# Kernel optimization log

Hardware: AMD Instinct MI355X
Metric: run time of the kernel (lower is better)

The kernel has to match this reference:

```python
import jax, jax.numpy as jnp
import numpy as np

N_NODES = 50000
N_EDGES = 800000
R = 3          # relations
D_IN = 96
D_HID = 96
D_OUT = 64


def setup_inputs() -> dict:
    key = jax.random.key(0)
    ks = jax.random.split(key, 10)
    s_in = 1.0 / np.sqrt(D_IN)
    s_hid = 1.0 / np.sqrt(D_HID)
    return {
        "x": jax.random.normal(ks[0], (N_NODES, D_IN), jnp.float32),
        "src": jax.random.randint(ks[1], (R, N_EDGES), 0, N_NODES, jnp.int32),
        "dst": jax.random.randint(ks[2], (R, N_EDGES), 0, N_NODES, jnp.int32),
        "Ws1": jax.random.normal(ks[3], (R, D_IN, D_HID), jnp.float32) * s_in,
        "Wn1": jax.random.normal(ks[4], (R, D_IN, D_HID), jnp.float32) * s_in,
        "b1": jnp.zeros((R, D_HID), jnp.float32),
        "Ws2": jax.random.normal(ks[5], (R, D_HID, D_OUT), jnp.float32) * s_hid,
        "Wn2": jax.random.normal(ks[6], (R, D_HID, D_OUT), jnp.float32) * s_hid,
        "b2": jnp.zeros((R, D_OUT), jnp.float32),
    }


def reference(x, src, dst, Ws1, Wn1, b1, Ws2, Wn2, b2):
    N = x.shape[0]
    # in-degree per relation, clamped to 1 (DGL zero-in-degree convention)
    deg = jax.vmap(lambda d: jax.ops.segment_sum(
        jnp.ones(d.shape[0], x.dtype), d, num_segments=N))(dst)        # [R, N]
    inv_deg = (1.0 / jnp.maximum(deg, 1.0))[..., None]                 # [R, N, 1]

    def sage_layer(h, Ws, Wn, b):
        # gather src feats, mean-aggregate onto dst, per relation
        neigh = jax.vmap(lambda s, d: jax.ops.segment_sum(
            h[s], d, num_segments=N))(src, dst) * inv_deg              # [R, N, Din]
        out = jnp.tanh(
            jnp.einsum('nd,rdh->rnh', h, Ws)
            + jnp.einsum('rnd,rdh->rnh', neigh, Wn)
            + b[:, None, :])                                           # [R, N, H]
        return out.mean(axis=0)  # HeteroGraphConv aggregate='mean'

    h1 = sage_layer(x, Ws1, Wn1, b1)
    return sage_layer(h1, Ws2, Wn2, b2)
```

## Files before the change

### kernel.cpp

```cpp
#include <hip/hip_runtime.h>
#include <hip/hip_bf16.h>

constexpr int NN   = 50000;
constexpr int NE   = 800000;
constexpr int NR   = 3;
constexpr int DIN  = 96;
constexpr int DH   = 96;
constexpr int DOUT = 64;
constexpr int SLOT = 48;
constexpr int ZROW = NN;

constexpr float QS_X   = 127.0f / 5.5f;
constexpr float STEP_X = 5.5f / 127.0f;
constexpr float STEP_H = 1.0f / 127.0f;

constexpr int NBUCK   = 196;
constexpr int LCAP    = 56;
constexpr int P1B     = 256;
constexpr int CHUNK   = NE / P1B;
constexpr int BSTRIDE = 3200;
constexpr int LSTRIDE = 200;

constexpr int SCAT_BLKS = NR * P1B;
constexpr int CONV_BLKS = (NN * 96 + 4095) / 4096;
constexpr int WT_ELEMS  = 2 * NR * DIN * DH + 2 * NR * DH * DOUT;
constexpr int WT_BLKS   = (WT_ELEMS + 511) / 512;
constexpr int PREP_GRID = SCAT_BLKS + CONV_BLKS + WT_BLKS;

typedef __attribute__((ext_vector_type(8))) short bf16x8;
typedef __attribute__((ext_vector_type(4))) float f32x4;
typedef __attribute__((ext_vector_type(4))) unsigned int uint4v;

__device__ __forceinline__ unsigned short f2b(float f) {
    unsigned int u = __float_as_uint(f);
    u += 0x7fffu + ((u >> 16) & 1u);
    return (unsigned short)(u >> 16);
}
__device__ __forceinline__ unsigned int pack2(float lo, float hi) {
    return (unsigned int)f2b(lo) | ((unsigned int)f2b(hi) << 16);
}
__device__ __forceinline__ unsigned int q8u(float f, float s) {
    int v = (int)lrintf(f * s);
    v = v < -127 ? -127 : (v > 127 ? 127 : v);
    return (unsigned int)(v + 128);
}

struct __align__(4) U3 { unsigned int x, y, z; };

__global__ __launch_bounds__(512)
void prep_kernel(const int* __restrict__ src,
                 const int* __restrict__ dst,
                 unsigned int* __restrict__ gbuck,
                 int* __restrict__ glofs,
                 const float* __restrict__ x,
                 unsigned short* __restrict__ xb,
                 unsigned char* __restrict__ xq,
                 unsigned short* __restrict__ h1b,
                 unsigned char* __restrict__ h1q,
                 const float* __restrict__ Ws1, const float* __restrict__ Wn1,
                 const float* __restrict__ Ws2, const float* __restrict__ Wn2,
                 unsigned short* __restrict__ wt)
{
    __shared__ unsigned int lbuf[NBUCK][LCAP];
    __shared__ int lcnt[NBUCK];
    __shared__ int sa[256], sb[256];
    __shared__ int lofs[NBUCK + 1];

    const int bid = blockIdx.x;
    const int tid = threadIdx.x;

    if (bid < SCAT_BLKS) {
        const int r = bid >> 8, c = bid & 255;
        for (int i = tid; i < NBUCK; i += 512) lcnt[i] = 0;
        __syncthreads();

        const int* sr = src + (size_t)r * NE + (size_t)c * CHUNK;
        const int* dr = dst + (size_t)r * NE + (size_t)c * CHUNK;
        for (int i = tid; i < CHUNK; i += 512) {
            int d = dr[i];
            int s = sr[i];
            int b = d >> 8;
            int pos = atomicAdd(&lcnt[b], 1);
            if (pos < LCAP)
                lbuf[b][pos] = ((unsigned int)(d & 255) << 16) | (unsigned int)s;
        }
        __syncthreads();

        if (tid < 256)
            sa[tid] = (tid < NBUCK) ? min(lcnt[tid], LCAP) : 0;
        __syncthreads();
        int* cur = sa; int* nxt = sb;
        for (int st = 1; st < 256; st <<= 1) {
            if (tid < 256) {
                int v = cur[tid];
                if (tid >= st) v += cur[tid - st];
                nxt[tid] = v;
            }
            __syncthreads();
            int* t2 = cur; cur = nxt; nxt = t2;
        }
        if (tid == 0) lofs[0] = 0;
        if (tid < NBUCK) lofs[tid + 1] = cur[tid];
        __syncthreads();

        if (tid < NBUCK + 1) glofs[(size_t)bid * LSTRIDE + tid] = lofs[tid];

        const int w = tid >> 6, l = tid & 63;
        unsigned int* gb = gbuck + (size_t)bid * BSTRIDE;
        for (int b = w; b < NBUCK; b += 8) {
            int cnt = min(lcnt[b], LCAP);
            if (l < cnt) gb[lofs[b] + l] = lbuf[b][l];
        }
    } else if (bid < SCAT_BLKS + CONV_BLKS) {
        const int rb = bid - SCAT_BLKS;
        if (rb == 0) {
            if (tid < 48) {
                reinterpret_cast<unsigned int*>(xb  + (size_t)ZROW * 96)[tid] = 0u;
            } else if (tid >= 64 && tid < 112) {
                reinterpret_cast<unsigned int*>(h1b + (size_t)ZROW * 96)[tid - 64] = 0u;
            } else if (tid >= 128 && tid < 152) {
                reinterpret_cast<unsigned int*>(xq  + (size_t)ZROW * 96)[tid - 128] = 0x80808080u;
            } else if (tid >= 192 && tid < 216) {
                reinterpret_cast<unsigned int*>(h1q + (size_t)ZROW * 96)[tid - 192] = 0x80808080u;
            }
        }
        int i = (rb * 512 + tid) * 8;
        if (i < NN * 96) {
            float4 a = *reinterpret_cast<const float4*>(x + i);
            float4 b = *reinterpret_cast<const float4*>(x + i + 4);
            uint4 o;
            o.x = pack2(a.x, a.y);
            o.y = pack2(a.z, a.w);
            o.z = pack2(b.x, b.y);
            o.w = pack2(b.z, b.w);
            *reinterpret_cast<uint4*>(xb + i) = o;
            unsigned int qlo = q8u(a.x, QS_X) | (q8u(a.y, QS_X) << 8)
                             | (q8u(a.z, QS_X) << 16) | (q8u(a.w, QS_X) << 24);
            unsigned int qhi = q8u(b.x, QS_X) | (q8u(b.y, QS_X) << 8)
                             | (q8u(b.z, QS_X) << 16) | (q8u(b.w, QS_X) << 24);
            unsigned int* q = reinterpret_cast<unsigned int*>(xq + i);
            q[0] = qlo;
            q[1] = qhi;
        }
    } else {
        int g = (bid - SCAT_BLKS - CONV_BLKS) * 512 + tid;
        if (g < WT_ELEMS) {
            constexpr int SZ1 = NR * DIN * DH;
            constexpr int SZ2 = NR * DH * DOUT;
            const float* in;
            int idx, KD, ND;
            if (g < SZ1)                { in = Ws1; idx = g;                 KD = DIN; ND = DH; }
            else if (g < 2 * SZ1)       { in = Wn1; idx = g - SZ1;           KD = DIN; ND = DH; }
            else if (g < 2 * SZ1 + SZ2) { in = Ws2; idx = g - 2 * SZ1;       KD = DH;  ND = DOUT; }
            else                        { in = Wn2; idx = g - 2 * SZ1 - SZ2; KD = DH;  ND = DOUT; }
            int k = idx % KD;
            int rn = idx / KD;
            int n = rn % ND;
            int r = rn / ND;
            wt[g] = f2b(in[((size_t)r * KD + k) * ND + n]);
        }
    }
}

__global__ __launch_bounds__(512)
void bin_build_kernel(const unsigned int* __restrict__ gbuck,
                      const int* __restrict__ glofs,
                      unsigned short* __restrict__ slots,
                      int* __restrict__ deg)
{
    __shared__ unsigned short lslot[256][SLOT];
    __shared__ int lcnt[256];

    const int rb = blockIdx.x;
    const int r  = rb / NBUCK, b = rb - r * NBUCK;
    const int nbase = b * 256;
    int nb = NN - nbase; if (nb > 256) nb = 256;
    const int tid = threadIdx.x;

    unsigned int* ls32i = reinterpret_cast<unsigned int*>(&lslot[0][0]);
    for (int i = tid; i < 256 * SLOT / 2; i += 512) ls32i[i] = 0xC350C350u;
    for (int i = tid; i < 256; i += 512) lcnt[i] = 0;
    __syncthreads();

    const int blk  = tid >> 1;
    const int half = tid & 1;
    const int gblk = r * P1B + blk;
    int o0 = glofs[(size_t)gblk * LSTRIDE + b];
    int o1 = glofs[(size_t)gblk * LSTRIDE + b + 1];
    const unsigned int* run = gbuck + (size_t)gblk * BSTRIDE + o0;
    int cnt = o1 - o0;
    for (int i = half; i < cnt; i += 2) {
        unsigned int e = run[i];
        int nl = e >> 16;
        int pos = atomicAdd(&lcnt[nl], 1);
        if (pos < SLOT) lslot[nl][pos] = (unsigned short)(e & 0xffffu);
    }
    __syncthreads();

    for (int j = tid; j < nb; j += 512) deg[r * NN + nbase + j] = lcnt[j];

    const unsigned int* ls32 = reinterpret_cast<const unsigned int*>(&lslot[0][0]);
    unsigned int* gs32 = reinterpret_cast<unsigned int*>(
        slots + ((size_t)r * NN + nbase) * SLOT);
    const int tot = nb * (SLOT / 2);
    for (int i = tid; i < tot; i += 512) gs32[i] = ls32[i];
}

__global__ __launch_bounds__(256)
void agg_q8_kernel(const unsigned char* __restrict__ Hq,
                   const unsigned short* __restrict__ slots,
                   const int* __restrict__ deg,
                   unsigned int* __restrict__ aggb,
                   float step)
{
    int gid = blockIdx.x * 256 + threadIdx.x;
    int grp = gid >> 3, t = gid & 7;
    if (grp >= NR * NN) return;
    const uint4v* sl4 = reinterpret_cast<const uint4v*>(slots + (size_t)grp * SLOT);
    int e = deg[grp];
    if (e > SLOT) e = SLOT;

    uint4v iv0 = __builtin_nontemporal_load(sl4 + 0);
    uint4v iv1 = __builtin_nontemporal_load(sl4 + 1);
    uint4v iv2 = __builtin_nontemporal_load(sl4 + 2);
    uint4v iv3 = __builtin_nontemporal_load(sl4 + 3);

    const unsigned char* Tb = Hq + 12 * t;
    unsigned int l0 = 0, h0 = 0, l1 = 0, h1 = 0, l2 = 0, h2 = 0;
    const unsigned int M = 0x00FF00FFu;

#define DO8Q(V)                                                                \
    {                                                                          \
        unsigned int i0 = (V).x & 0xffffu, i1 = (V).x >> 16;                   \
        unsigned int i2 = (V).y & 0xffffu, i3 = (V).y >> 16;                   \
        unsigned int i4 = (V).z & 0xffffu, i5 = (V).z >> 16;                   \
        unsigned int i6 = (V).w & 0xffffu, i7 = (V).w >> 16;                   \
        U3 g0 = *reinterpret_cast<const U3*>(Tb + (size_t)i0 * 96);            \
        U3 g1 = *reinterpret_cast<const U3*>(Tb + (size_t)i1 * 96);            \
        U3 g2 = *reinterpret_cast<const U3*>(Tb + (size_t)i2 * 96);            \
        U3 g3 = *reinterpret_cast<const U3*>(Tb + (size_t)i3 * 96);            \
        U3 g4 = *reinterpret_cast<const U3*>(Tb + (size_t)i4 * 96);            \
        U3 g5 = *reinterpret_cast<const U3*>(Tb + (size_t)i5 * 96);            \
        U3 g6 = *reinterpret_cast<const U3*>(Tb + (size_t)i6 * 96);            \
        U3 g7 = *reinterpret_cast<const U3*>(Tb + (size_t)i7 * 96);            \
        l0 += g0.x & M; h0 += (g0.x >> 8) & M;                                 \
        l1 += g0.y & M; h1 += (g0.y >> 8) & M;                                 \
        l2 += g0.z & M; h2 += (g0.z >> 8) & M;                                 \
        l0 += g1.x & M; h0 += (g1.x >> 8) & M;                                 \
        l1 += g1.y & M; h1 += (g1.y >> 8) & M;                                 \
        l2 += g1.z & M; h2 += (g1.z >> 8) & M;                                 \
        l0 += g2.x & M; h0 += (g2.x >> 8) & M;                                 \
        l1 += g2.y & M; h1 += (g2.y >> 8) & M;                                 \
        l2 += g2.z & M; h2 += (g2.z >> 8) & M;                                 \
        l0 += g3.x & M; h0 += (g3.x >> 8) & M;                                 \
        l1 += g3.y & M; h1 += (g3.y >> 8) & M;                                 \
        l2 += g3.z & M; h2 += (g3.z >> 8) & M;                                 \
        l0 += g4.x & M; h0 += (g4.x >> 8) & M;                                 \
        l1 += g4.y & M; h1 += (g4.y >> 8) & M;                                 \
        l2 += g4.z & M; h2 += (g4.z >> 8) & M;                                 \
        l0 += g5.x & M; h0 += (g5.x >> 8) & M;                                 \
        l1 += g5.y & M; h1 += (g5.y >> 8) & M;                                 \
        l2 += g5.z & M; h2 += (g5.z >> 8) & M;                                 \
        l0 += g6.x & M; h0 += (g6.x >> 8) & M;                                 \
        l1 += g6.y & M; h1 += (g6.y >> 8) & M;                                 \
        l2 += g6.z & M; h2 += (g6.z >> 8) & M;                                 \
        l0 += g7.x & M; h0 += (g7.x >> 8) & M;                                 \
        l1 += g7.y & M; h1 += (g7.y >> 8) & M;                                 \
        l2 += g7.z & M; h2 += (g7.z >> 8) & M;                                 \
    }

    int nb8 = (e + 7) >> 3;
    if (nb8 > 0) DO8Q(iv0);
    if (nb8 > 1) DO8Q(iv1);
    if (nb8 > 2) DO8Q(iv2);
    if (nb8 > 3) DO8Q(iv3);
    for (int i = 32; i < e; i += 8) {
        uint4v v = __builtin_nontemporal_load(sl4 + (i >> 3));
        DO8Q(v);
    }
#undef DO8Q

    const int bias = 128 * 8 * nb8;
    const float inv = step / (float)(e > 0 ? e : 1);
    float f0  = (float)((int)(l0 & 0xFFFFu) - bias) * inv;
    float f1  = (float)((int)(h0 & 0xFFFFu) - bias) * inv;
    float f2  = (float)((int)(l0 >> 16)     - bias) * inv;
    float f3  = (float)((int)(h0 >> 16)     - bias) * inv;
    float f4  = (float)((int)(l1 & 0xFFFFu) - bias) * inv;
    float f5  = (float)((int)(h1 & 0xFFFFu) - bias) * inv;
    float f6  = (float)((int)(l1 >> 16)     - bias) * inv;
    float f7  = (float)((int)(h1 >> 16)     - bias) * inv;
    float f8  = (float)((int)(l2 & 0xFFFFu) - bias) * inv;
    float f9  = (float)((int)(h2 & 0xFFFFu) - bias) * inv;
    float f10 = (float)((int)(l2 >> 16)     - bias) * inv;
    float f11 = (float)((int)(h2 >> 16)     - bias) * inv;

    unsigned int* o = aggb + (size_t)grp * 48 + t * 6;
    o[0] = pack2(f0, f1);
    o[1] = pack2(f2, f3);
    o[2] = pack2(f4, f5);
    o[3] = pack2(f6, f7);
    o[4] = pack2(f8, f9);
    o[5] = pack2(f10, f11);
}

template <int NOUT, bool OUT16, int CSPLIT>
__global__ __launch_bounds__(256)
void mfma_layer_kernel(const unsigned short* __restrict__ Hb,
                       const unsigned short* __restrict__ aggb,
                       const unsigned short* __restrict__ Wts,
                       const unsigned short* __restrict__ Wtn,
                       const float* __restrict__ bias,
                       unsigned short* __restrict__ o16,
                       unsigned char* __restrict__ oq8,
                       float* __restrict__ o32)
{
    const int nb   = blockIdx.x / CSPLIT;
    const int cblk = blockIdx.x - nb * CSPLIT;
    const int w    = threadIdx.x >> 6;
    const int l    = threadIdx.x & 63;
    const int n0   = nb * 64 + w * 16;
    const int arow = l & 15, asel = l >> 4;
    int na = n0 + arow;
    if (na > NN - 1) na = NN - 1;

    bf16x8 ax[3], ag[NR][3];
    {
        const unsigned short* xr = Hb + (size_t)na * 96 + asel * 8;
        #pragma unroll
        for (int kb = 0; kb < 3; ++kb)
            ax[kb] = *reinterpret_cast<const bf16x8*>(xr + kb * 32);
        #pragma unroll
        for (int r = 0; r < NR; ++r) {
            const unsigned short* gr = aggb + ((size_t)r * NN + na) * 96 + asel * 8;
            #pragma unroll
            for (int kb = 0; kb < 3; ++kb)
                ag[r][kb] = *reinterpret_cast<const bf16x8*>(gr + kb * 32);
        }
    }

    constexpr int NC  = NOUT / 16;
    constexpr int NCC = NC / CSPLIT;
    #pragma unroll
    for (int ci = 0; ci < NCC; ++ci) {
        const int c = cblk * NCC + ci;
        f32x4 acc[NR];
        #pragma unroll
        for (int r = 0; r < NR; ++r) acc[r] = (f32x4){0.f, 0.f, 0.f, 0.f};

        #pragma unroll
        for (int r = 0; r < NR; ++r) {
            const unsigned short* bs = Wts + ((size_t)r * NOUT + c * 16 + arow) * 96 + asel * 8;
            const unsigned short* bn = Wtn + ((size_t)r * NOUT + c * 16 + arow) * 96 + asel * 8;
            #pragma unroll
            for (int kb = 0; kb < 3; ++kb) {
                acc[r] = __builtin_amdgcn_mfma_f32_16x16x32_bf16(
                    ax[kb], *reinterpret_cast<const bf16x8*>(bs + kb * 32), acc[r], 0, 0, 0);
                acc[r] = __builtin_amdgcn_mfma_f32_16x16x32_bf16(
                    ag[r][kb], *reinterpret_cast<const bf16x8*>(bn + kb * 32), acc[r], 0, 0, 0);
            }
        }

        const int col = c * 16 + arow;
        const float b0 = bias[col];
        const float b1 = bias[NOUT + col];
        const float b2 = bias[2 * NOUT + col];
        #pragma unroll
        for (int j = 0; j < 4; ++j) {
            int node = n0 + asel * 4 + j;
            if (node < NN) {
                float v = (tanhf(acc[0][j] + b0) + tanhf(acc[1][j] + b1)
                         + tanhf(acc[2][j] + b2)) * (1.0f / 3.0f);
                if (OUT16) {
                    o16[(size_t)node * 96 + col] = f2b(v);
                    oq8[(size_t)node * 96 + col] = (unsigned char)q8u(v, 127.0f);
                } else {
                    o32[(size_t)node * DOUT + col] = v;
                }
            }
        }
    }
}

extern "C" void kernel_launch(void* const* d_in, const int* in_sizes, int n_in,
                              void* d_out, int out_size, void* d_ws, size_t ws_size,
                              hipStream_t stream)
{
    const float* x   = (const float*)d_in[0];
    const int*   src = (const int*)d_in[1];
    const int*   dst = (const int*)d_in[2];
    const float* Ws1 = (const float*)d_in[3];
    const float* Wn1 = (const float*)d_in[4];
    const float* b1  = (const float*)d_in[5];
    const float* Ws2 = (const float*)d_in[6];
    const float* Wn2 = (const float*)d_in[7];
    const float* b2  = (const float*)d_in[8];
    float* out = (float*)d_out;

    char* ws = (char*)d_ws;
    size_t o = 0;
    auto alloc = [&](size_t bytes) {
        size_t p = o;
        o += (bytes + 255) & ~(size_t)255;
        return p;
    };
    int* deg = (int*)(ws + alloc((size_t)NR * NN * 4));
    unsigned short* slots = (unsigned short*)(ws + alloc((size_t)NR * NN * SLOT * 2));
    unsigned short* xb = (unsigned short*)(ws + alloc((size_t)(NN + 1) * 96 * 2));
    unsigned char* xq = (unsigned char*)(ws + alloc((size_t)(NN + 1) * 96));
    unsigned short* h1b = (unsigned short*)(ws + alloc((size_t)(NN + 1) * 96 * 2));
    unsigned char* h1q = (unsigned char*)(ws + alloc((size_t)(NN + 1) * 96));
    char* aggregion = ws + alloc((size_t)NR * NN * 96 * 2);
    unsigned short* wt = (unsigned short*)(ws + alloc((size_t)WT_ELEMS * 2));
    unsigned short* wt1s = wt;
    unsigned short* wt1n = wt1s + NR * DIN * DH;
    unsigned short* wt2s = wt1n + NR * DIN * DH;
    unsigned short* wt2n = wt2s + NR * DH * DOUT;

    unsigned int* gbuck = (unsigned int*)aggregion;
    int* glofs = (int*)(aggregion + (size_t)NR * P1B * BSTRIDE * 4);
    unsigned short* aggb = (unsigned short*)aggregion;

    prep_kernel<<<PREP_GRID, 512, 0, stream>>>(
        src, dst, gbuck, glofs, x, xb, xq, h1b, h1q, Ws1, Wn1, Ws2, Wn2, wt);
    bin_build_kernel<<<NR * NBUCK, 512, 0, stream>>>(gbuck, glofs, slots, deg);

    constexpr int AGG_GRID  = (NR * NN * 8 + 255) / 256;
    constexpr int NBLKN     = (NN + 63) / 64;

    agg_q8_kernel<<<AGG_GRID, 256, 0, stream>>>(
        xq, slots, deg, (unsigned int*)aggb, STEP_X);
    mfma_layer_kernel<DH, true, 3><<<NBLKN * 3, 256, 0, stream>>>(
        xb, aggb, wt1s, wt1n, b1, h1b, h1q, (float*)nullptr);

    agg_q8_kernel<<<AGG_GRID, 256, 0, stream>>>(
        h1q, slots, deg, (unsigned int*)aggb, STEP_H);
    mfma_layer_kernel<DOUT, false, 2><<<NBLKN * 2, 256, 0, stream>>>(
        h1b, aggb, wt2s, wt2n, b2, (unsigned short*)nullptr, (unsigned char*)nullptr, out);
}
```

Before: 175.2 us.

## Stage weights in LDS per relation and compute all output columns per block

```diff
diff --git a/kernel.cpp b/kernel.cpp
--- a/kernel.cpp
+++ b/kernel.cpp
@@ -27,6 +27,8 @@
 constexpr int WT_BLKS   = (WT_ELEMS + 511) / 512;
 constexpr int PREP_GRID = SCAT_BLKS + CONV_BLKS + WT_BLKS;
 
+constexpr int LPAD = 104;
+
 typedef __attribute__((ext_vector_type(8))) short bf16x8;
 typedef __attribute__((ext_vector_type(4))) float f32x4;
 typedef __attribute__((ext_vector_type(4))) unsigned int uint4v;
@@ -43,6 +45,11 @@
     int v = (int)lrintf(f * s);
     v = v < -127 ? -127 : (v > 127 ? 127 : v);
     return (unsigned int)(v + 128);
+}
+__device__ __forceinline__ float fast_tanh(float x) {
+    x = fminf(fmaxf(x, -30.0f), 30.0f);
+    float e = exp2f(x * 2.8853900817779268f);
+    return (e - 1.0f) * __builtin_amdgcn_rcpf(e + 1.0f);
 }
 
 struct __align__(4) U3 { unsigned int x, y, z; };
@@ -304,7 +311,7 @@
     o[5] = pack2(f10, f11);
 }
 
-template <int NOUT, bool OUT16, int CSPLIT>
+template <int NOUT, bool OUT16>
 __global__ __launch_bounds__(256)
 void mfma_layer_kernel(const unsigned short* __restrict__ Hb,
                        const unsigned short* __restrict__ aggb,
@@ -315,11 +322,13 @@
                        unsigned char* __restrict__ oq8,
                        float* __restrict__ o32)
 {
-    const int nb   = blockIdx.x / CSPLIT;
-    const int cblk = blockIdx.x - nb * CSPLIT;
-    const int w    = threadIdx.x >> 6;
-    const int l    = threadIdx.x & 63;
-    const int n0   = nb * 64 + w * 16;
+    __shared__ unsigned short lds_s[NOUT * LPAD];
+    __shared__ unsigned short lds_n[NOUT * LPAD];
+
+    const int tid  = threadIdx.x;
+    const int w    = tid >> 6;
+    const int l    = tid & 63;
+    const int n0   = blockIdx.x * 64 + w * 16;
     const int arow = l & 15, asel = l >> 4;
     int na = n0 + arow;
     if (na > NN - 1) na = NN - 1;
@@ -339,38 +348,59 @@
         }
     }
 
-    constexpr int NC  = NOUT / 16;
-    constexpr int NCC = NC / CSPLIT;
+    constexpr int NC = NOUT / 16;
+    float res[NC][4];
     #pragma unroll
-    for (int ci = 0; ci < NCC; ++ci) {
-        const int c = cblk * NCC + ci;
-        f32x4 acc[NR];
+    for (int c = 0; c < NC; ++c)
         #pragma unroll
-        for (int r = 0; r < NR; ++r) acc[r] = (f32x4){0.f, 0.f, 0.f, 0.f};
+        for (int j = 0; j < 4; ++j) res[c][j] = 0.f;
+
+    unsigned int* ls32 = reinterpret_cast<unsigned int*>(lds_s);
+    unsigned int* ln32 = reinterpret_cast<unsigned int*>(lds_n);
+
+    for (int r = 0; r < NR; ++r) {
+        if (r > 0) __syncthreads();
+        const unsigned int* srcs = reinterpret_cast<const unsigned int*>(
+            Wts + (size_t)r * NOUT * 96);
+        const unsigned int* srcn = reinterpret_cast<const unsigned int*>(
+            Wtn + (size_t)r * NOUT * 96);
+        constexpr int NDW = NOUT * 48;
+        for (int i = tid; i < NDW; i += 256) {
+            int row = i / 48, c2 = i - row * 48;
+            ls32[row * (LPAD / 2) + c2] = srcs[i];
+            ln32[row * (LPAD / 2) + c2] = srcn[i];
+        }
+        __syncthreads();
 
         #pragma unroll
-        for (int r = 0; r < NR; ++r) {
-            const unsigned short* bs = Wts + ((size_t)r * NOUT + c * 16 + arow) * 96 + asel * 8;
-            const unsigned short* bn = Wtn + ((size_t)r * NOUT + c * 16 + arow) * 96 + asel * 8;
+        for (int c = 0; c < NC; ++c) {
+            const int col = c * 16 + arow;
+            const unsigned short* bs = lds_s + (size_t)col * LPAD + asel * 8;
+            const unsigned short* bn = lds_n + (size_t)col * LPAD + asel * 8;
+            f32x4 acc = (f32x4){0.f, 0.f, 0.f, 0.f};
             #pragma unroll
             for (int kb = 0; kb < 3; ++kb) {
-                acc[r] = __builtin_amdgcn_mfma_f32_16x16x32_bf16(
-                    ax[kb], *reinterpret_cast<const bf16x8*>(bs + kb * 32), acc[r], 0, 0, 0);
-                acc[r] = __builtin_amdgcn_mfma_f32_16x16x32_bf16(
-                    ag[r][kb], *reinterpret_cast<const bf16x8*>(bn + kb * 32), acc[r], 0, 0, 0);
+                acc = __builtin_amdgcn_mfma_f32_16x16x32_bf16(
+                    ax[kb], *reinterpret_cast<const bf16x8*>(bs + kb * 32), acc, 0, 0, 0);
+                acc = __builtin_amdgcn_mfma_f32_16x16x32_bf16(
+                    ag[r][kb], *reinterpret_cast<const bf16x8*>(bn + kb * 32), acc, 0, 0, 0);
             }
-        }
-
+            const float bb = bias[r * NOUT + col];
+            #pragma unroll
+            for (int j = 0; j < 4; ++j)
+                res[c][j] += fast_tanh(acc[j] + bb);
+        }
+    }
+
+    const float third = 1.0f / 3.0f;
+    #pragma unroll
+    for (int c = 0; c < NC; ++c) {
         const int col = c * 16 + arow;
-        const float b0 = bias[col];
-        const float b1 = bias[NOUT + col];
-        const float b2 = bias[2 * NOUT + col];
         #pragma unroll
         for (int j = 0; j < 4; ++j) {
             int node = n0 + asel * 4 + j;
             if (node < NN) {
-                float v = (tanhf(acc[0][j] + b0) + tanhf(acc[1][j] + b1)
-                         + tanhf(acc[2][j] + b2)) * (1.0f / 3.0f);
+                float v = res[c][j] * third;
                 if (OUT16) {
                     o16[(size_t)node * 96 + col] = f2b(v);
                     oq8[(size_t)node * 96 + col] = (unsigned char)q8u(v, 127.0f);
@@ -430,11 +460,11 @@
 
     agg_q8_kernel<<<AGG_GRID, 256, 0, stream>>>(
         xq, slots, deg, (unsigned int*)aggb, STEP_X);
-    mfma_layer_kernel<DH, true, 3><<<NBLKN * 3, 256, 0, stream>>>(
+    mfma_layer_kernel<DH, true><<<NBLKN, 256, 0, stream>>>(
         xb, aggb, wt1s, wt1n, b1, h1b, h1q, (float*)nullptr);
 
     agg_q8_kernel<<<AGG_GRID, 256, 0, stream>>>(
         h1q, slots, deg, (unsigned int*)aggb, STEP_H);
-    mfma_layer_kernel<DOUT, false, 2><<<NBLKN * 2, 256, 0, stream>>>(
+    mfma_layer_kernel<DOUT, false><<<NBLKN, 256, 0, stream>>>(
         h1b, aggb, wt2s, wt2n, b2, (unsigned short*)nullptr, (unsigned char*)nullptr, out);
 }
```

Measured after the change: 173.3 us, median of 2. About the same (-1.1%).
